# Performance work log

Hardware: AMD Instinct MI355X
Metric: run time of the kernel (lower is better)

## Reference

```python
import jax, jax.numpy as jnp
import numpy as np


def _chamfer(array1, array2):
    # array1: [B, N, 3], array2: [B, M, 3]
    sq1 = jnp.sum(array1 * array1, axis=-1)            # [B, N]
    sq2 = jnp.sum(array2 * array2, axis=-1)            # [B, M]
    inner = jnp.einsum('bnd,bmd->bnm', array1, array2)  # [B, N, M]
    d = sq1[:, :, None] + sq2[:, None, :] - 2.0 * inner  # [B, N, M]
    d = jnp.maximum(d, 0.0)  # clamp tiny negatives from cancellation
    dist1 = jnp.min(d, axis=2)  # [B, N] nearest in array2 for each pt in array1
    dist2 = jnp.min(d, axis=1)  # [B, M] nearest in array1 for each pt in array2
    return dist1, dist2


def setup_inputs() -> dict:
    key = jax.random.key(0)
    k1, k2 = jax.random.split(key)
    B, N, M = 8, 4096, 4096
    array1 = jax.random.normal(k1, (B, N, 3), dtype=jnp.float32)
    array2 = jax.random.normal(k2, (B, M, 3), dtype=jnp.float32)
    return {"array1": array1, "array2": array2}


def reference(array1, array2):
    dist1, dist2 = _chamfer(array1, array2)
    return jnp.mean(dist1) + jnp.mean(dist2)
```

## Files before the change

kernel.cpp:

```cpp
#include <hip/hip_runtime.h>
#include <math.h>

#define BATCH   8
#define NPTS    4096
#define TOTAL   (BATCH * NPTS)
#define NTILES  (TOTAL / 16)
#define MSPLIT  4
#define ITERS   (256 / MSPLIT)
#define NWAVES  (2 * BATCH * 128 * MSPLIT)
#define BUFSZ   ((size_t)(NTILES * 64 + 64))

typedef __attribute__((ext_vector_type(8))) short bfrag;
typedef __attribute__((ext_vector_type(4))) float ffrag;

__device__ __forceinline__ unsigned short bf16_rne(float f) {
    unsigned u = __float_as_uint(f);
    return (unsigned short)((u + 0x7FFFu + ((u >> 16) & 1u)) >> 16);
}
__device__ __forceinline__ float bf16f(unsigned short h) {
    return __uint_as_float(((unsigned)h) << 16);
}


__global__ __launch_bounds__(256)
void pack_kernel(const float* __restrict__ a1, const float* __restrict__ a2,
                 uint4* __restrict__ frags) {
    const int w    = blockIdx.x * 4 + (threadIdx.x >> 6);
    const int lane = threadIdx.x & 63;
    const int koct = lane >> 4;
    const int idx  = lane & 15;
    const int buf  = w >> 11;
    const int tile = w & (NTILES - 1);
    const bool isA = (buf < 2);
    const float* __restrict__ src = (buf & 1) ? a2 : a1;
    const int p = tile * 16 + idx;
    float x = src[3 * p + 0], y = src[3 * p + 1], z = src[3 * p + 2];
    float s = fmaf(x, x, fmaf(y, y, z * z));
    const unsigned short ONE = 0x3F80;
    unsigned short v[8] = {0, 0, 0, 0, 0, 0, 0, 0};
    if (isA) {
        if (koct == 0) {
            unsigned short xh = bf16_rne(x), xl = bf16_rne(x - bf16f(xh));
            unsigned short yh = bf16_rne(y), yl = bf16_rne(y - bf16f(yh));
            unsigned short zh = bf16_rne(z);
            v[0]=xh; v[1]=xh; v[2]=xl; v[3]=yh; v[4]=yh; v[5]=yl; v[6]=zh; v[7]=zh;
        } else if (koct == 1) {
            unsigned short zh = bf16_rne(z), zl = bf16_rne(z - bf16f(zh));
            unsigned short sh = bf16_rne(s), sl = bf16_rne(s - bf16f(sh));
            v[0]=zl; v[1]=ONE; v[2]=ONE; v[3]=sh; v[4]=sl;
        }
    } else {
        float X = -2.f * x, Y = -2.f * y, Z = -2.f * z;
        if (koct == 0) {
            unsigned short Xh = bf16_rne(X), Xl = bf16_rne(X - bf16f(Xh));
            unsigned short Yh = bf16_rne(Y), Yl = bf16_rne(Y - bf16f(Yh));
            unsigned short Zh = bf16_rne(Z), Zl = bf16_rne(Z - bf16f(Zh));
            v[0]=Xh; v[1]=Xl; v[2]=Xh; v[3]=Yh; v[4]=Yl; v[5]=Yh; v[6]=Zh; v[7]=Zl;
        } else if (koct == 1) {
            unsigned short Zh = bf16_rne(Z);
            unsigned short Wh = bf16_rne(s), Wl = bf16_rne(s - bf16f(Wh));
            v[0]=Zh; v[1]=Wh; v[2]=Wl; v[3]=ONE; v[4]=ONE;
        }
    }
    uint4 pk;
    pk.x = (unsigned)v[0] | ((unsigned)v[1] << 16);
    pk.y = (unsigned)v[2] | ((unsigned)v[3] << 16);
    pk.z = (unsigned)v[4] | ((unsigned)v[5] << 16);
    pk.w = (unsigned)v[6] | ((unsigned)v[7] << 16);
    frags[(size_t)buf * BUFSZ + (size_t)tile * 64 + lane] = pk;
}

__global__ __launch_bounds__(256, 8)
void chamfer_mfma_kernel(const uint4* __restrict__ frags,
                         unsigned* __restrict__ dist) {
    const int w    = blockIdx.x * 4 + (threadIdx.x >> 6);
    const int lane = threadIdx.x & 63;
    const int dir    = w >> 12;
    const int sub    = w & 4095;
    const int batch  = sub >> 9;
    const int rem    = sub & 511;
    const int msplit = rem >> 7;
    const int nwave  = rem & 127;

    const int ntile0 = batch * 256 + nwave * 2;
    const int mt0    = batch * 256 + msplit * ITERS;

    const bfrag* __restrict__ Af = (const bfrag*)(frags + (size_t)(dir ? 1 : 0) * BUFSZ);
    const bfrag* __restrict__ Bf = (const bfrag*)(frags + (size_t)(dir ? 2 : 3) * BUFSZ);
    unsigned* __restrict__ dst = dist + (size_t)dir * TOTAL;

    bfrag a0 = Af[(size_t)ntile0 * 64 + lane];
    bfrag a1 = Af[(size_t)(ntile0 + 1) * 64 + lane];
    const bfrag* __restrict__ Bp = Bf + (size_t)mt0 * 64 + lane;

    const ffrag zero = {0.f, 0.f, 0.f, 0.f};
    float racc[8];
    #pragma unroll
    for (int q = 0; q < 8; q++) racc[q] = __builtin_inff();

    bfrag bcur = Bp[0];
    #pragma unroll 4
    for (int it = 0; it < ITERS; it++) {
        bfrag bnxt = Bp[(size_t)(it + 1) * 64];
        ffrag c0 = __builtin_amdgcn_mfma_f32_16x16x32_bf16(a0, bcur, zero, 0, 0, 0);
        ffrag c1 = __builtin_amdgcn_mfma_f32_16x16x32_bf16(a1, bcur, zero, 0, 0, 0);
        #pragma unroll
        for (int q = 0; q < 4; q++) racc[q]     = fminf(racc[q],     c0[q]);
        #pragma unroll
        for (int q = 0; q < 4; q++) racc[4 + q] = fminf(racc[4 + q], c1[q]);
        bcur = bnxt;
    }

    #pragma unroll
    for (int q = 0; q < 8; q++) {
        float v = racc[q];
        v = fminf(v, __shfl_xor(v, 1));
        v = fminf(v, __shfl_xor(v, 2));
        v = fminf(v, __shfl_xor(v, 4));
        v = fminf(v, __shfl_xor(v, 8));
        racc[q] = fmaxf(v, 0.f);
    }
    if ((lane & 15) == 0) {
        const int quad = lane >> 4;
        unsigned* __restrict__ b0 = dst + ntile0 * 16 + quad * 4;
        #pragma unroll
        for (int q = 0; q < 4; q++) atomicMin(b0 + q, __float_as_uint(racc[q]));
        unsigned* __restrict__ b1 = dst + (ntile0 + 1) * 16 + quad * 4;
        #pragma unroll
        for (int q = 0; q < 4; q++) atomicMin(b1 + q, __float_as_uint(racc[4 + q]));
    }
}

__global__ __launch_bounds__(1024)
void reduce_kernel(const float* __restrict__ dist, float* __restrict__ out) {
    const float4* __restrict__ dv = (const float4*)dist;
    float s = 0.0f;
    #pragma unroll
    for (int i = 0; i < (2 * TOTAL / 4) / 1024; i++) {
        float4 v = dv[i * 1024 + threadIdx.x];
        s += (v.x + v.y) + (v.z + v.w);
    }
    #pragma unroll
    for (int off = 32; off > 0; off >>= 1) s += __shfl_down(s, off, 64);
    __shared__ float wsum[16];
    if ((threadIdx.x & 63) == 0) wsum[threadIdx.x >> 6] = s;
    __syncthreads();
    if (threadIdx.x < 16) {
        float v = wsum[threadIdx.x];
        #pragma unroll
        for (int off = 8; off > 0; off >>= 1) v += __shfl_down(v, off, 16);
        if (threadIdx.x == 0) out[0] = v * (1.0f / (float)TOTAL);
    }
}

extern "C" void kernel_launch(void* const* d_in, const int* in_sizes, int n_in,
                              void* d_out, int out_size, void* d_ws, size_t ws_size,
                              hipStream_t stream) {
    const float* a1 = (const float*)d_in[0];
    const float* a2 = (const float*)d_in[1];
    float* out = (float*)d_out;

    uint4*    frags = (uint4*)d_ws;
    unsigned* dist  = (unsigned*)((char*)d_ws + 4 * BUFSZ * sizeof(uint4));

    pack_kernel<<<(4 * NTILES) / 4, 256, 0, stream>>>(a1, a2, frags);
    chamfer_mfma_kernel<<<NWAVES / 4, 256, 0, stream>>>(frags, dist);
    reduce_kernel<<<1, 1024, 0, stream>>>((const float*)dist, out);
}
```

Measured before the change: 85.21 us.

## Register-block 8 A fragments per wave and process two B tiles per iteration

Each wave now keeps 8 A-side 16-point fragments in registers instead of 2, so every B fragment loaded from memory feeds 8 MFMAs. The M dimension is split 8 ways and the loop consumes two B fragments per step, with a combined min update. This reduces B-fragment load traffic per MFMA and per-iteration loop overhead. The cost is more registers, lower occupancy (launch bounds 4), fewer waves, and slightly larger buffer padding for prefetch overrun.

```diff
diff --git a/kernel.cpp b/kernel.cpp
--- a/kernel.cpp
+++ b/kernel.cpp
@@ -5,10 +5,11 @@
 #define NPTS    4096
 #define TOTAL   (BATCH * NPTS)
 #define NTILES  (TOTAL / 16)
-#define MSPLIT  4
+#define AFRAGS  8
+#define MSPLIT  8
 #define ITERS   (256 / MSPLIT)
-#define NWAVES  (2 * BATCH * 128 * MSPLIT)
-#define BUFSZ   ((size_t)(NTILES * 64 + 64))
+#define NWAVES  (2 * BATCH * (256 / AFRAGS) * MSPLIT)
+#define BUFSZ   ((size_t)(NTILES * 64 + 256))
 
 typedef __attribute__((ext_vector_type(8))) short bfrag;
 typedef __attribute__((ext_vector_type(4))) float ffrag;
@@ -70,64 +71,76 @@
     frags[(size_t)buf * BUFSZ + (size_t)tile * 64 + lane] = pk;
 }
 
-__global__ __launch_bounds__(256, 8)
+__global__ __launch_bounds__(256, 4)
 void chamfer_mfma_kernel(const uint4* __restrict__ frags,
                          unsigned* __restrict__ dist) {
     const int w    = blockIdx.x * 4 + (threadIdx.x >> 6);
     const int lane = threadIdx.x & 63;
-    const int dir    = w >> 12;
-    const int sub    = w & 4095;
-    const int batch  = sub >> 9;
-    const int rem    = sub & 511;
-    const int msplit = rem >> 7;
-    const int nwave  = rem & 127;
+    const int dir    = w >> 11;
+    const int sub    = w & 2047;
+    const int batch  = sub >> 8;
+    const int rem    = sub & 255;
+    const int msplit = rem >> 5;
+    const int nwave  = rem & 31;
 
-    const int ntile0 = batch * 256 + nwave * 2;
+    const int ntile0 = batch * 256 + nwave * AFRAGS;
     const int mt0    = batch * 256 + msplit * ITERS;
 
     const bfrag* __restrict__ Af = (const bfrag*)(frags + (size_t)(dir ? 1 : 0) * BUFSZ);
     const bfrag* __restrict__ Bf = (const bfrag*)(frags + (size_t)(dir ? 2 : 3) * BUFSZ);
     unsigned* __restrict__ dst = dist + (size_t)dir * TOTAL;
 
-    bfrag a0 = Af[(size_t)ntile0 * 64 + lane];
-    bfrag a1 = Af[(size_t)(ntile0 + 1) * 64 + lane];
+    bfrag a[AFRAGS];
+    #pragma unroll
+    for (int f = 0; f < AFRAGS; f++)
+        a[f] = Af[(size_t)(ntile0 + f) * 64 + lane];
     const bfrag* __restrict__ Bp = Bf + (size_t)mt0 * 64 + lane;
 
     const ffrag zero = {0.f, 0.f, 0.f, 0.f};
-    float racc[8];
+    float racc[AFRAGS][4];
     #pragma unroll
-    for (int q = 0; q < 8; q++) racc[q] = __builtin_inff();
+    for (int f = 0; f < AFRAGS; f++)
+        #pragma unroll
+        for (int q = 0; q < 4; q++) racc[f][q] = __builtin_inff();
 
-    bfrag bcur = Bp[0];
-    #pragma unroll 4
-    for (int it = 0; it < ITERS; it++) {
-        bfrag bnxt = Bp[(size_t)(it + 1) * 64];
-        ffrag c0 = __builtin_amdgcn_mfma_f32_16x16x32_bf16(a0, bcur, zero, 0, 0, 0);
-        ffrag c1 = __builtin_amdgcn_mfma_f32_16x16x32_bf16(a1, bcur, zero, 0, 0, 0);
+    bfrag b0 = Bp[0];
+    bfrag b1 = Bp[64];
+    for (int it = 0; it < ITERS; it += 2) {
+        bfrag n0 = Bp[(size_t)(it + 2) * 64];
+        bfrag n1 = Bp[(size_t)(it + 3) * 64];
         #pragma unroll
-        for (int q = 0; q < 4; q++) racc[q]     = fminf(racc[q],     c0[q]);
-        #pragma unroll
-        for (int q = 0; q < 4; q++) racc[4 + q] = fminf(racc[4 + q], c1[q]);
-        bcur = bnxt;
+        for (int f = 0; f < AFRAGS; f++) {
+            ffrag ca = __builtin_amdgcn_mfma_f32_16x16x32_bf16(a[f], b0, zero, 0, 0, 0);
+            ffrag cb = __builtin_amdgcn_mfma_f32_16x16x32_bf16(a[f], b1, zero, 0, 0, 0);
+            #pragma unroll
+            for (int q = 0; q < 4; q++)
+                racc[f][q] = fminf(fminf(ca[q], cb[q]), racc[f][q]);
+        }
+        b0 = n0;
+        b1 = n1;
     }
 
     #pragma unroll
-    for (int q = 0; q < 8; q++) {
-        float v = racc[q];
-        v = fminf(v, __shfl_xor(v, 1));
-        v = fminf(v, __shfl_xor(v, 2));
-        v = fminf(v, __shfl_xor(v, 4));
-        v = fminf(v, __shfl_xor(v, 8));
-        racc[q] = fmaxf(v, 0.f);
+    for (int f = 0; f < AFRAGS; f++) {
+        #pragma unroll
+        for (int q = 0; q < 4; q++) {
+            float v = racc[f][q];
+            v = fminf(v, __shfl_xor(v, 1));
+            v = fminf(v, __shfl_xor(v, 2));
+            v = fminf(v, __shfl_xor(v, 4));
+            v = fminf(v, __shfl_xor(v, 8));
+            racc[f][q] = fmaxf(v, 0.f);
+        }
     }
     if ((lane & 15) == 0) {
         const int quad = lane >> 4;
-        unsigned* __restrict__ b0 = dst + ntile0 * 16 + quad * 4;
         #pragma unroll
-        for (int q = 0; q < 4; q++) atomicMin(b0 + q, __float_as_uint(racc[q]));
-        unsigned* __restrict__ b1 = dst + (ntile0 + 1) * 16 + quad * 4;
-        #pragma unroll
-        for (int q = 0; q < 4; q++) atomicMin(b1 + q, __float_as_uint(racc[4 + q]));
+        for (int f = 0; f < AFRAGS; f++) {
+            unsigned* __restrict__ b = dst + (ntile0 + f) * 16 + quad * 4;
+            #pragma unroll
+            for (int q = 0; q < 4; q++)
+                atomicMin(b + q, __float_as_uint(racc[f][q]));
+        }
     }
 }
 
```

After: 85.42 us. About the same (+0.3%).
